# Kernel tuning notes

Hardware: AMD Instinct MI355X
Metric: run time of the kernel (lower is better)

## Reference

```python
import jax, jax.numpy as jnp
import numpy as np

N = 50000      # nodes
F_IN = 512     # input features
HID = 128      # hidden
CLS = 64       # classes
E = 800000     # edges (avg degree 16)
EPS = 1e-5


def setup_inputs() -> dict:
    key = jax.random.key(0)
    k = jax.random.split(key, 6)
    x = jax.random.normal(k[0], (N, F_IN), jnp.float32)
    edge_index = jax.random.randint(k[1], (2, E), 0, N, dtype=jnp.int32)
    W1 = jax.random.normal(k[2], (F_IN, HID), jnp.float32) / np.float32(np.sqrt(F_IN))
    b1 = jnp.zeros((HID,), jnp.float32)
    W2 = jax.random.normal(k[3], (HID, CLS), jnp.float32) / np.float32(np.sqrt(HID))
    b2 = jnp.zeros((CLS,), jnp.float32)
    return {"x": x, "edge_index": edge_index, "W1": W1, "b1": b1, "W2": W2, "b2": b2}


def bin_active(x):
    # BinActive(scalar=True): per-node sign binarization scaled by mean |x| over features
    return jnp.sign(x) * jnp.mean(jnp.abs(x), axis=1, keepdims=True)


def bin_weight(w):
    # binarized weight with per-output-channel scaling (XNOR-style)
    return jnp.sign(w) * jnp.mean(jnp.abs(w), axis=0, keepdims=True)


def gcn_norm(edge_index, n):
    # add self-loops, symmetric D^-1/2 (A+I) D^-1/2 normalization (cached in original)
    loops = jnp.arange(n, dtype=edge_index.dtype)
    row = jnp.concatenate([edge_index[0], loops])  # source
    col = jnp.concatenate([edge_index[1], loops])  # target
    deg = jax.ops.segment_sum(jnp.ones(row.shape[0], jnp.float32), col, num_segments=n)
    dinv = jnp.where(deg > 0, jax.lax.rsqrt(jnp.maximum(deg, 1.0)), 0.0)
    return row, col, dinv[row] * dinv[col]


def bigcn_conv(x, W, b, row, col, norm, n):
    h = x @ bin_weight(W)                                   # [n, out]
    msg = norm[:, None] * h[row]                            # gather + scale, [E+n, out]
    return jax.ops.segment_sum(msg, col, num_segments=n) + b


def reference(x, edge_index, W1, b1, W2, b2):
    n = x.shape[0]
    # BatchNorm1d(affine=False), batch statistics (biased var)
    mu = jnp.mean(x, axis=0)
    var = jnp.var(x, axis=0)
    x = (x - mu) * jax.lax.rsqrt(var + EPS)
    row, col, norm = gcn_norm(edge_index, n)
    # layer loop: BinActive -> (dropout is identity in eval) -> BiGCNConv
    x = bigcn_conv(bin_active(x), W1, b1, row, col, norm, n)
    x = bigcn_conv(bin_active(x), W2, b2, row, col, norm, n)
    return jax.nn.log_softmax(x, axis=1)
```

## Files before the change

### kernel.cpp

```cpp
#include <hip/hip_runtime.h>

typedef unsigned long long u64;

#define F_IN 512
#define HID 128
#define CLS 64
#define EPS 1e-5f
#define NSB 512

__global__ __launch_bounds__(256) void prep_k(const float4* __restrict__ x4,
                                              float* __restrict__ psum,
                                              float* __restrict__ psq,
                                              int n, int rpb,
                                              const int* __restrict__ col,
                                              int* __restrict__ deg, int e, int nbdeg,
                                              const float* __restrict__ W1,
                                              u64* __restrict__ sig1,
                                              float* __restrict__ beta1,
                                              const float* __restrict__ W2,
                                              ulonglong2* __restrict__ sigw2,
                                              float* __restrict__ beta2) {
    __shared__ float red[256][9];
    int b = blockIdx.x;
    int tid = threadIdx.x;
    if (b < NSB) {
        int c4 = tid & 127;
        int half = tid >> 7;
        int r0 = b * rpb;
        int r1 = min(n, r0 + rpb);
        float s0=0.f,s1=0.f,s2=0.f,s3=0.f,q0=0.f,q1=0.f,q2=0.f,q3=0.f;
#pragma unroll 4
        for (int r = r0 + half; r < r1; r += 2) {
            float4 v = x4[(size_t)r * 128 + c4];
            s0 += v.x; q0 += v.x * v.x;
            s1 += v.y; q1 += v.y * v.y;
            s2 += v.z; q2 += v.z * v.z;
            s3 += v.w; q3 += v.w * v.w;
        }
        red[tid][0]=s0; red[tid][1]=s1; red[tid][2]=s2; red[tid][3]=s3;
        red[tid][4]=q0; red[tid][5]=q1; red[tid][6]=q2; red[tid][7]=q3;
        __syncthreads();
        if (half == 0) {
            int c = c4 * 4;
            float* os = &psum[(size_t)b * 512 + c];
            float* oq = &psq [(size_t)b * 512 + c];
            os[0] = s0 + red[c4+128][0]; os[1] = s1 + red[c4+128][1];
            os[2] = s2 + red[c4+128][2]; os[3] = s3 + red[c4+128][3];
            oq[0] = q0 + red[c4+128][4]; oq[1] = q1 + red[c4+128][5];
            oq[2] = q2 + red[c4+128][6]; oq[3] = q3 + red[c4+128][7];
        }
    } else if (b < NSB + nbdeg) {
        int i = (b - NSB) * 256 + tid;
        if (i < e) atomicAdd(&deg[col[i]], 1);
    } else if (b < NSB + nbdeg + 32) {
        int wave = tid >> 6, l = tid & 63;
        int j = (b - NSB - nbdeg) * 4 + wave;
        float asum = 0.f;
#pragma unroll
        for (int jw = 0; jw < 8; ++jw) {
            int f = (jw < 4) ? (4*l + jw) : (256 + 4*l + (jw - 4));
            float v = W1[(size_t)f * HID + j];
            asum += fabsf(v);
            u64 bb = __ballot(v > 0.0f);
            if (l == 0) sig1[jw * HID + j] = bb;
        }
        for (int m = 32; m >= 1; m >>= 1) asum += __shfl_xor(asum, m);
        if (l == 0) beta1[j] = asum * (1.0f / 512.0f);
    } else {
        int wave = tid >> 6, l = tid & 63;
        int j = (b - NSB - nbdeg - 32) * 4 + wave;
        float v0 = W2[(size_t)(2 * l) * CLS + j];
        float v1 = W2[(size_t)(2 * l + 1) * CLS + j];
        float asum = fabsf(v0) + fabsf(v1);
        u64 s0 = __ballot(v0 > 0.0f);
        u64 s1 = __ballot(v1 > 0.0f);
        for (int m = 32; m >= 1; m >>= 1) asum += __shfl_xor(asum, m);
        if (l == 0) {
            ulonglong2 t; t.x = s0; t.y = s1;
            sigw2[j] = t;
            beta2[j] = asum * (1.0f / 128.0f);
        }
    }
}

__global__ __launch_bounds__(256) void mid_k(const float* __restrict__ psum,
                                             const float* __restrict__ psq,
                                             float* __restrict__ mu,
                                             float* __restrict__ rinv, int n,
                                             const int* __restrict__ deg,
                                             int* __restrict__ bsum) {
    __shared__ float reds[256], redq[256];
    __shared__ int lds[256];
    int b = blockIdx.x;
    int t = threadIdx.x;
    if (b < 16) {
        int cc = t & 31;
        int bs = t >> 5;
        int c = b * 32 + cc;
        float s = 0.f, q = 0.f;
#pragma unroll 4
        for (int p = bs; p < NSB; p += 8) {
            s += psum[(size_t)p * 512 + c];
            q += psq [(size_t)p * 512 + c];
        }
        reds[t] = s; redq[t] = q;
        __syncthreads();
        if (bs == 0) {
#pragma unroll
            for (int u = 1; u < 8; ++u) { s += reds[cc + 32*u]; q += redq[cc + 32*u]; }
            float m = s / (float)n;
            float v = q / (float)n - m * m;
            mu[c] = m;
            rinv[c] = rsqrtf(v + EPS);
        }
    } else {
        int blk = b - 16;
        int i = blk * 256 + t;
        lds[t] = (i < n) ? deg[i] : 0;
        __syncthreads();
        for (int s = 128; s > 0; s >>= 1) {
            if (t < s) lds[t] += lds[t + s];
            __syncthreads();
        }
        if (t == 0) bsum[blk] = lds[0];
    }
}

__global__ __launch_bounds__(256) void scan_bsum_k(const int* __restrict__ bsum,
                                                   int* __restrict__ boff, int nb) {
    __shared__ int lds[256];
    int t = threadIdx.x;
    int v = (t < nb) ? bsum[t] : 0;
    lds[t] = v;
    __syncthreads();
    for (int s = 1; s < 256; s <<= 1) {
        int add = (t >= s) ? lds[t - s] : 0;
        __syncthreads();
        lds[t] += add;
        __syncthreads();
    }
    if (t < nb) boff[t] = lds[t] - v;
}

__global__ __launch_bounds__(256) void scan_final_k(const int* __restrict__ deg,
                                                    const int* __restrict__ boff,
                                                    int* __restrict__ offs,
                                                    int* __restrict__ cursor,
                                                    float* __restrict__ dinv, int n) {
    __shared__ int lds[256];
    int t = threadIdx.x;
    int i = blockIdx.x * 256 + t;
    int v = (i < n) ? deg[i] : 0;
    lds[t] = v;
    __syncthreads();
    for (int s = 1; s < 256; s <<= 1) {
        int add = (t >= s) ? lds[t - s] : 0;
        __syncthreads();
        lds[t] += add;
        __syncthreads();
    }
    int excl = lds[t] - v + boff[blockIdx.x];
    if (i < n) {
        offs[i] = excl; cursor[i] = excl;
        dinv[i] = rsqrtf((float)v + 1.0f);
    }
}

__global__ __launch_bounds__(256) void main1_k(const float4* __restrict__ x4,
                                               const float4* __restrict__ mu4,
                                               const float4* __restrict__ rinv4,
                                               const u64* __restrict__ sigW,
                                               float* __restrict__ a1,
                                               short2* __restrict__ dots, int n, int nbin,
                                               const int* __restrict__ row,
                                               const int* __restrict__ col,
                                               const float* __restrict__ dinv,
                                               int* __restrict__ cursor,
                                               int2* __restrict__ csr, int e) {
    int b = blockIdx.x;
    int tid = threadIdx.x;
    if (b < nbin) {
        int wave = tid >> 6, l = tid & 63;
        int i = b * 4 + wave;
        if (i >= n) return;
        const float4* xr = x4 + (size_t)i * 128;
        float4 va = xr[l], vb = xr[64 + l];
        float4 ma = mu4[l], mb = mu4[64 + l];
        float4 ra = rinv4[l], rb = rinv4[64 + l];
        float t0 = va.x - ma.x, t1 = va.y - ma.y, t2 = va.z - ma.z, t3 = va.w - ma.w;
        float t4 = vb.x - mb.x, t5 = vb.y - mb.y, t6 = vb.z - mb.z, t7 = vb.w - mb.w;
        float asum = fabsf(t0)*ra.x + fabsf(t1)*ra.y + fabsf(t2)*ra.z + fabsf(t3)*ra.w
                   + fabsf(t4)*rb.x + fabsf(t5)*rb.y + fabsf(t6)*rb.z + fabsf(t7)*rb.w;
        u64 sx[8];
        sx[0] = __ballot(t0 > 0.f); sx[1] = __ballot(t1 > 0.f);
        sx[2] = __ballot(t2 > 0.f); sx[3] = __ballot(t3 > 0.f);
        sx[4] = __ballot(t4 > 0.f); sx[5] = __ballot(t5 > 0.f);
        sx[6] = __ballot(t6 > 0.f); sx[7] = __ballot(t7 > 0.f);
        for (int m = 32; m >= 1; m >>= 1) asum += __shfl_xor(asum, m);
        if (l == 0) a1[i] = asum * (1.0f / 512.0f);
        int c0 = 0, c1 = 0;
#pragma unroll
        for (int w = 0; w < 8; ++w) {
            c0 += __popcll(sx[w] ^ sigW[w * HID + 2*l]);
            c1 += __popcll(sx[w] ^ sigW[w * HID + 2*l + 1]);
        }
        dots[(size_t)i * 64 + l] = make_short2((short)(512 - 2*c0), (short)(512 - 2*c1));
    } else {
        int i = (b - nbin) * 256 + tid;
        if (i < e) {
            int r = row[i], c = col[i];
            int p = atomicAdd(&cursor[c], 1);
            float w = dinv[r] * dinv[c];
            csr[p] = make_int2(r, __float_as_int(w));
        }
    }
}

__global__ __launch_bounds__(256) void agg1_fused_k(const short2* __restrict__ dots,
                                                    const float* __restrict__ a1,
                                                    const int2* __restrict__ csr,
                                                    const int* __restrict__ offs,
                                                    const int* __restrict__ deg,
                                                    const float* __restrict__ dinv,
                                                    const float2* __restrict__ beta1_2,
                                                    const float2* __restrict__ b1_2,
                                                    u64* __restrict__ sig2x,
                                                    float* __restrict__ a2v, int n) {
    int tid = threadIdx.x;
    int wave = tid >> 6, l = tid & 63;
    int i = blockIdx.x * 4 + wave;
    if (i >= n) return;
    float di = dinv[i];
    float ts = di * di * a1[i];
    short2 ds = dots[(size_t)i * 64 + l];
    float acc0 = ts * (float)ds.x;
    float acc1 = ts * (float)ds.y;
    int off = offs[i], d = deg[i];
    int k = 0;
    for (; k + 8 <= d; k += 8) {
        int2 ee[8]; float tt[8]; short2 dd[8];
#pragma unroll
        for (int u = 0; u < 8; ++u) ee[u] = csr[off + k + u];
#pragma unroll
        for (int u = 0; u < 8; ++u) tt[u] = __int_as_float(ee[u].y) * a1[ee[u].x];
#pragma unroll
        for (int u = 0; u < 8; ++u) dd[u] = dots[(size_t)ee[u].x * 64 + l];
#pragma unroll
        for (int u = 0; u < 8; ++u) {
            acc0 += tt[u] * (float)dd[u].x;
            acc1 += tt[u] * (float)dd[u].y;
        }
    }
    for (; k < d; ++k) {
        int2 ew = csr[off + k];
        float t = __int_as_float(ew.y) * a1[ew.x];
        short2 dv = dots[(size_t)ew.x * 64 + l];
        acc0 += t * (float)dv.x;
        acc1 += t * (float)dv.y;
    }
    float2 be = beta1_2[l], bb = b1_2[l];
    acc0 = be.x * acc0 + bb.x;
    acc1 = be.y * acc1 + bb.y;
    float asum = fabsf(acc0) + fabsf(acc1);
    for (int m = 32; m >= 1; m >>= 1) asum += __shfl_xor(asum, m);
    u64 s0 = __ballot(acc0 > 0.f);
    u64 s1 = __ballot(acc1 > 0.f);
    if (l == 0) {
        ulonglong2 pk; pk.x = s0; pk.y = s1;
        *(ulonglong2*)&sig2x[2 * (size_t)i] = pk;
        a2v[i] = asum * (1.0f / 128.0f);
    }
}

__global__ __launch_bounds__(256) void agg2_pop_k(const u64* __restrict__ sig2x,
                                                  const float* __restrict__ a2v,
                                                  const int2* __restrict__ csr,
                                                  const int* __restrict__ offs,
                                                  const int* __restrict__ deg,
                                                  const float* __restrict__ dinv,
                                                  const ulonglong2* __restrict__ sigw2,
                                                  const float* __restrict__ beta2,
                                                  const float* __restrict__ b2,
                                                  float* __restrict__ out, int n) {
    int tid = threadIdx.x;
    int wave = tid >> 6, l = tid & 63;
    int i = blockIdx.x * 4 + wave;
    if (i >= n) return;
    ulonglong2 wsig = sigw2[l];
    float bet = beta2[l], bias = b2[l];
    float di = dinv[i];
    float ts = di * di * a2v[i];
    ulonglong2 ss = *(const ulonglong2*)&sig2x[2 * (size_t)i];
    int dp = __popcll(ss.x ^ wsig.x) + __popcll(ss.y ^ wsig.y);
    float acc = ts * (float)(128 - 2 * dp);
    int off = offs[i], d = deg[i];
    int k = 0;
    for (; k + 8 <= d; k += 8) {
        int2 ee[8]; float tt[8]; ulonglong2 gg[8];
#pragma unroll
        for (int u = 0; u < 8; ++u) ee[u] = csr[off + k + u];
#pragma unroll
        for (int u = 0; u < 8; ++u) tt[u] = __int_as_float(ee[u].y) * a2v[ee[u].x];
#pragma unroll
        for (int u = 0; u < 8; ++u) gg[u] = *(const ulonglong2*)&sig2x[2 * (size_t)ee[u].x];
#pragma unroll
        for (int u = 0; u < 8; ++u) {
            int p = __popcll(gg[u].x ^ wsig.x) + __popcll(gg[u].y ^ wsig.y);
            acc += tt[u] * (float)(128 - 2 * p);
        }
    }
    for (; k < d; ++k) {
        int2 ew = csr[off + k];
        ulonglong2 gs = *(const ulonglong2*)&sig2x[2 * (size_t)ew.x];
        float t = __int_as_float(ew.y) * a2v[ew.x];
        int p = __popcll(gs.x ^ wsig.x) + __popcll(gs.y ^ wsig.y);
        acc += t * (float)(128 - 2 * p);
    }
    float o = bet * acc + bias;
    float m = o;
    for (int k2 = 32; k2 >= 1; k2 >>= 1) m = fmaxf(m, __shfl_xor(m, k2));
    float ev = __expf(o - m);
    float s = ev;
    for (int k2 = 32; k2 >= 1; k2 >>= 1) s += __shfl_xor(s, k2);
    out[(size_t)i * CLS + l] = o - m - __logf(s);
}

extern "C" void kernel_launch(void* const* d_in, const int* in_sizes, int n_in,
                              void* d_out, int out_size, void* d_ws, size_t ws_size,
                              hipStream_t stream) {
    const float* x  = (const float*)d_in[0];
    const int*   ei = (const int*)d_in[1];
    const float* W1 = (const float*)d_in[2];
    const float* b1 = (const float*)d_in[3];
    const float* W2 = (const float*)d_in[4];
    const float* b2 = (const float*)d_in[5];
    float* out = (float*)d_out;

    const int n = in_sizes[0] / F_IN;
    const int e = in_sizes[1] / 2;
    const int* row = ei;
    const int* col = ei + e;

    char* w = (char*)d_ws;
    size_t off = 0;
    auto alloc = [&](size_t bytes) {
        void* p = w + off;
        off += (bytes + 255) & ~(size_t)255;
        return p;
    };
    int*   deg    = (int*)alloc((size_t)n * 4);
    size_t zero_bytes = off;
    float* psum   = (float*)alloc((size_t)NSB * 512 * 4);
    float* psq    = (float*)alloc((size_t)NSB * 512 * 4);
    float* mu     = (float*)alloc(F_IN * 4);
    float* rinv   = (float*)alloc(F_IN * 4);
    float* dinv   = (float*)alloc((size_t)n * 4);
    float* beta1  = (float*)alloc(HID * 4);
    u64*   sig1   = (u64*)alloc(HID * 8 * 8);
    ulonglong2* sigw2 = (ulonglong2*)alloc(CLS * 16);
    float* beta2  = (float*)alloc(CLS * 4);
    int*   offs   = (int*)alloc((size_t)n * 4);
    int*   cursor = (int*)alloc((size_t)n * 4);
    int*   bsum   = (int*)alloc(256 * 4);
    int*   boff   = (int*)alloc(256 * 4);
    int2*  csr    = (int2*)alloc((size_t)e * 8);
    short2* dots  = (short2*)alloc((size_t)n * 64 * 4);
    float* a1     = (float*)alloc((size_t)n * 4);
    u64*   sig2x  = (u64*)alloc((size_t)n * 2 * 8);
    float* a2v    = (float*)alloc((size_t)n * 4);
    (void)ws_size;

    hipMemsetAsync(deg, 0, zero_bytes, stream);

    int rpb = (n + NSB - 1) / NSB;
    int nbdeg = (e + 255) / 256;
    int nb = (n + 255) / 256;
    int nbin = (n + 3) / 4;

    prep_k<<<NSB + nbdeg + 32 + 16, 256, 0, stream>>>(
        (const float4*)x, psum, psq, n, rpb,
        col, deg, e, nbdeg,
        W1, sig1, beta1, W2, sigw2, beta2);

    mid_k<<<16 + nb, 256, 0, stream>>>(psum, psq, mu, rinv, n, deg, bsum);
    scan_bsum_k<<<1, 256, 0, stream>>>(bsum, boff, nb);
    scan_final_k<<<nb, 256, 0, stream>>>(deg, boff, offs, cursor, dinv, n);

    main1_k<<<nbin + nbdeg, 256, 0, stream>>>(
        (const float4*)x, (const float4*)mu, (const float4*)rinv, sig1, a1, dots, n, nbin,
        row, col, dinv, cursor, csr, e);

    agg1_fused_k<<<nbin, 256, 0, stream>>>(dots, a1, csr, offs, deg, dinv,
                                           (const float2*)beta1, (const float2*)b1,
                                           sig2x, a2v, n);
    agg2_pop_k<<<nbin, 256, 0, stream>>>(sig2x, a2v, csr, offs, deg, dinv,
                                         sigw2, beta2, b2, out, n);
}
```

Baseline: 360.8 us.

## Fold dinv into per-node scale, shrink CSR to int indices, vectorize edge loops

The symmetric normalization dinv[r]*dinv[c] is factored out. The source factor is folded into the per-node scale arrays (pa1/pa2), and the target factor is applied once after aggregation. Because of this the CSR stores only source indices as 4-byte ints instead of int2 pairs, which halves edge-list traffic in both aggregation passes. Degree counting and CSR fill now process four edges per thread with int4 loads, and degree is read from offs[i+1]-offs[i]. The risk is a small change in floating-point rounding order and an extra offs entry written by scan_final_k.

```diff
diff --git a/kernel.cpp b/kernel.cpp
--- a/kernel.cpp
+++ b/kernel.cpp
@@ -50,8 +50,17 @@
             oq[2] = q2 + red[c4+128][6]; oq[3] = q3 + red[c4+128][7];
         }
     } else if (b < NSB + nbdeg) {
-        int i = (b - NSB) * 256 + tid;
-        if (i < e) atomicAdd(&deg[col[i]], 1);
+        int i4 = (b - NSB) * 256 + tid;
+        int base = i4 * 4;
+        if (base + 3 < e) {
+            int4 cc = *(const int4*)&col[base];
+            atomicAdd(&deg[cc.x], 1);
+            atomicAdd(&deg[cc.y], 1);
+            atomicAdd(&deg[cc.z], 1);
+            atomicAdd(&deg[cc.w], 1);
+        } else {
+            for (int i = base; i < e; ++i) atomicAdd(&deg[col[i]], 1);
+        }
     } else if (b < NSB + nbdeg + 32) {
         int wave = tid >> 6, l = tid & 63;
         int j = (b - NSB - nbdeg) * 4 + wave;
@@ -163,6 +172,8 @@
     if (i < n) {
         offs[i] = excl; cursor[i] = excl;
         dinv[i] = rsqrtf((float)v + 1.0f);
+    } else if (i == n) {
+        offs[n] = excl;
     }
 }
 
@@ -170,13 +181,13 @@
                                                const float4* __restrict__ mu4,
                                                const float4* __restrict__ rinv4,
                                                const u64* __restrict__ sigW,
-                                               float* __restrict__ a1,
+                                               const float* __restrict__ dinv,
+                                               float* __restrict__ pa1,
                                                short2* __restrict__ dots, int n, int nbin,
                                                const int* __restrict__ row,
                                                const int* __restrict__ col,
-                                               const float* __restrict__ dinv,
                                                int* __restrict__ cursor,
-                                               int2* __restrict__ csr, int e) {
+                                               int* __restrict__ csr, int e) {
     int b = blockIdx.x;
     int tid = threadIdx.x;
     if (b < nbin) {
@@ -197,7 +208,7 @@
         sx[4] = __ballot(t4 > 0.f); sx[5] = __ballot(t5 > 0.f);
         sx[6] = __ballot(t6 > 0.f); sx[7] = __ballot(t7 > 0.f);
         for (int m = 32; m >= 1; m >>= 1) asum += __shfl_xor(asum, m);
-        if (l == 0) a1[i] = asum * (1.0f / 512.0f);
+        if (l == 0) pa1[i] = dinv[i] * asum * (1.0f / 512.0f);
         int c0 = 0, c1 = 0;
 #pragma unroll
         for (int w = 0; w < 8; ++w) {
@@ -206,45 +217,51 @@
         }
         dots[(size_t)i * 64 + l] = make_short2((short)(512 - 2*c0), (short)(512 - 2*c1));
     } else {
-        int i = (b - nbin) * 256 + tid;
-        if (i < e) {
-            int r = row[i], c = col[i];
-            int p = atomicAdd(&cursor[c], 1);
-            float w = dinv[r] * dinv[c];
-            csr[p] = make_int2(r, __float_as_int(w));
+        int i4 = (b - nbin) * 256 + tid;
+        int base = i4 * 4;
+        if (base + 3 < e) {
+            int4 rr = *(const int4*)&row[base];
+            int4 cc = *(const int4*)&col[base];
+            csr[atomicAdd(&cursor[cc.x], 1)] = rr.x;
+            csr[atomicAdd(&cursor[cc.y], 1)] = rr.y;
+            csr[atomicAdd(&cursor[cc.z], 1)] = rr.z;
+            csr[atomicAdd(&cursor[cc.w], 1)] = rr.w;
+        } else {
+            for (int i = base; i < e; ++i)
+                csr[atomicAdd(&cursor[col[i]], 1)] = row[i];
         }
     }
 }
 
 __global__ __launch_bounds__(256) void agg1_fused_k(const short2* __restrict__ dots,
-                                                    const float* __restrict__ a1,
-                                                    const int2* __restrict__ csr,
+                                                    const float* __restrict__ pa1,
+                                                    const int* __restrict__ csr,
                                                     const int* __restrict__ offs,
-                                                    const int* __restrict__ deg,
                                                     const float* __restrict__ dinv,
                                                     const float2* __restrict__ beta1_2,
                                                     const float2* __restrict__ b1_2,
                                                     u64* __restrict__ sig2x,
-                                                    float* __restrict__ a2v, int n) {
+                                                    float* __restrict__ pa2, int n) {
     int tid = threadIdx.x;
     int wave = tid >> 6, l = tid & 63;
     int i = blockIdx.x * 4 + wave;
     if (i >= n) return;
     float di = dinv[i];
-    float ts = di * di * a1[i];
     short2 ds = dots[(size_t)i * 64 + l];
-    float acc0 = ts * (float)ds.x;
-    float acc1 = ts * (float)ds.y;
-    int off = offs[i], d = deg[i];
+    float p_i = pa1[i];
+    float acc0 = p_i * (float)ds.x;
+    float acc1 = p_i * (float)ds.y;
+    int off = offs[i];
+    int d = offs[i + 1] - off;
     int k = 0;
     for (; k + 8 <= d; k += 8) {
-        int2 ee[8]; float tt[8]; short2 dd[8];
-#pragma unroll
-        for (int u = 0; u < 8; ++u) ee[u] = csr[off + k + u];
-#pragma unroll
-        for (int u = 0; u < 8; ++u) tt[u] = __int_as_float(ee[u].y) * a1[ee[u].x];
-#pragma unroll
-        for (int u = 0; u < 8; ++u) dd[u] = dots[(size_t)ee[u].x * 64 + l];
+        int rr[8]; float tt[8]; short2 dd[8];
+#pragma unroll
+        for (int u = 0; u < 8; ++u) rr[u] = csr[off + k + u];
+#pragma unroll
+        for (int u = 0; u < 8; ++u) tt[u] = pa1[rr[u]];
+#pragma unroll
+        for (int u = 0; u < 8; ++u) dd[u] = dots[(size_t)rr[u] * 64 + l];
 #pragma unroll
         for (int u = 0; u < 8; ++u) {
             acc0 += tt[u] * (float)dd[u].x;
@@ -252,15 +269,15 @@
         }
     }
     for (; k < d; ++k) {
-        int2 ew = csr[off + k];
-        float t = __int_as_float(ew.y) * a1[ew.x];
-        short2 dv = dots[(size_t)ew.x * 64 + l];
+        int r = csr[off + k];
+        float t = pa1[r];
+        short2 dv = dots[(size_t)r * 64 + l];
         acc0 += t * (float)dv.x;
         acc1 += t * (float)dv.y;
     }
     float2 be = beta1_2[l], bb = b1_2[l];
-    acc0 = be.x * acc0 + bb.x;
-    acc1 = be.y * acc1 + bb.y;
+    acc0 = be.x * (di * acc0) + bb.x;
+    acc1 = be.y * (di * acc1) + bb.y;
     float asum = fabsf(acc0) + fabsf(acc1);
     for (int m = 32; m >= 1; m >>= 1) asum += __shfl_xor(asum, m);
     u64 s0 = __ballot(acc0 > 0.f);
@@ -268,15 +285,14 @@
     if (l == 0) {
         ulonglong2 pk; pk.x = s0; pk.y = s1;
         *(ulonglong2*)&sig2x[2 * (size_t)i] = pk;
-        a2v[i] = asum * (1.0f / 128.0f);
+        pa2[i] = di * asum * (1.0f / 128.0f);
     }
 }
 
 __global__ __launch_bounds__(256) void agg2_pop_k(const u64* __restrict__ sig2x,
-                                                  const float* __restrict__ a2v,
-                                                  const int2* __restrict__ csr,
+                                                  const float* __restrict__ pa2,
+                                                  const int* __restrict__ csr,
                                                   const int* __restrict__ offs,
-                                                  const int* __restrict__ deg,
                                                   const float* __restrict__ dinv,
                                                   const ulonglong2* __restrict__ sigw2,
                                                   const float* __restrict__ beta2,
@@ -289,20 +305,21 @@
     ulonglong2 wsig = sigw2[l];
     float bet = beta2[l], bias = b2[l];
     float di = dinv[i];
-    float ts = di * di * a2v[i];
+    float p_i = pa2[i];
     ulonglong2 ss = *(const ulonglong2*)&sig2x[2 * (size_t)i];
     int dp = __popcll(ss.x ^ wsig.x) + __popcll(ss.y ^ wsig.y);
-    float acc = ts * (float)(128 - 2 * dp);
-    int off = offs[i], d = deg[i];
+    float acc = p_i * (float)(128 - 2 * dp);
+    int off = offs[i];
+    int d = offs[i + 1] - off;
     int k = 0;
     for (; k + 8 <= d; k += 8) {
-        int2 ee[8]; float tt[8]; ulonglong2 gg[8];
-#pragma unroll
-        for (int u = 0; u < 8; ++u) ee[u] = csr[off + k + u];
-#pragma unroll
-        for (int u = 0; u < 8; ++u) tt[u] = __int_as_float(ee[u].y) * a2v[ee[u].x];
-#pragma unroll
-        for (int u = 0; u < 8; ++u) gg[u] = *(const ulonglong2*)&sig2x[2 * (size_t)ee[u].x];
+        int rr[8]; float tt[8]; ulonglong2 gg[8];
+#pragma unroll
+        for (int u = 0; u < 8; ++u) rr[u] = csr[off + k + u];
+#pragma unroll
+        for (int u = 0; u < 8; ++u) tt[u] = pa2[rr[u]];
+#pragma unroll
+        for (int u = 0; u < 8; ++u) gg[u] = *(const ulonglong2*)&sig2x[2 * (size_t)rr[u]];
 #pragma unroll
         for (int u = 0; u < 8; ++u) {
             int p = __popcll(gg[u].x ^ wsig.x) + __popcll(gg[u].y ^ wsig.y);
@@ -310,13 +327,13 @@
         }
     }
     for (; k < d; ++k) {
-        int2 ew = csr[off + k];
-        ulonglong2 gs = *(const ulonglong2*)&sig2x[2 * (size_t)ew.x];
-        float t = __int_as_float(ew.y) * a2v[ew.x];
+        int r = csr[off + k];
+        ulonglong2 gs = *(const ulonglong2*)&sig2x[2 * (size_t)r];
+        float t = pa2[r];
         int p = __popcll(gs.x ^ wsig.x) + __popcll(gs.y ^ wsig.y);
         acc += t * (float)(128 - 2 * p);
     }
-    float o = bet * acc + bias;
+    float o = bet * (di * acc) + bias;
     float m = o;
     for (int k2 = 32; k2 >= 1; k2 >>= 1) m = fmaxf(m, __shfl_xor(m, k2));
     float ev = __expf(o - m);
@@ -359,21 +376,22 @@
     u64*   sig1   = (u64*)alloc(HID * 8 * 8);
     ulonglong2* sigw2 = (ulonglong2*)alloc(CLS * 16);
     float* beta2  = (float*)alloc(CLS * 4);
-    int*   offs   = (int*)alloc((size_t)n * 4);
+    int*   offs   = (int*)alloc(((size_t)n + 1) * 4);
     int*   cursor = (int*)alloc((size_t)n * 4);
     int*   bsum   = (int*)alloc(256 * 4);
     int*   boff   = (int*)alloc(256 * 4);
-    int2*  csr    = (int2*)alloc((size_t)e * 8);
+    int*   csr    = (int*)alloc((size_t)e * 4);
     short2* dots  = (short2*)alloc((size_t)n * 64 * 4);
-    float* a1     = (float*)alloc((size_t)n * 4);
+    float* pa1    = (float*)alloc((size_t)n * 4);
     u64*   sig2x  = (u64*)alloc((size_t)n * 2 * 8);
-    float* a2v    = (float*)alloc((size_t)n * 4);
+    float* pa2    = (float*)alloc((size_t)n * 4);
     (void)ws_size;
 
     hipMemsetAsync(deg, 0, zero_bytes, stream);
 
     int rpb = (n + NSB - 1) / NSB;
-    int nbdeg = (e + 255) / 256;
+    int e4 = (e + 3) / 4;
+    int nbdeg = (e4 + 255) / 256;
     int nb = (n + 255) / 256;
     int nbin = (n + 3) / 4;
 
@@ -387,12 +405,13 @@
     scan_final_k<<<nb, 256, 0, stream>>>(deg, boff, offs, cursor, dinv, n);
 
     main1_k<<<nbin + nbdeg, 256, 0, stream>>>(
-        (const float4*)x, (const float4*)mu, (const float4*)rinv, sig1, a1, dots, n, nbin,
-        row, col, dinv, cursor, csr, e);
-
-    agg1_fused_k<<<nbin, 256, 0, stream>>>(dots, a1, csr, offs, deg, dinv,
+        (const float4*)x, (const float4*)mu, (const float4*)rinv, sig1,
+        dinv, pa1, dots, n, nbin,
+        row, col, cursor, csr, e);
+
+    agg1_fused_k<<<nbin, 256, 0, stream>>>(dots, pa1, csr, offs, dinv,
                                            (const float2*)beta1, (const float2*)b1,
-                                           sig2x, a2v, n);
-    agg2_pop_k<<<nbin, 256, 0, stream>>>(sig2x, a2v, csr, offs, deg, dinv,
+                                           sig2x, pa2, n);
+    agg2_pop_k<<<nbin, 256, 0, stream>>>(sig2x, pa2, csr, offs, dinv,
                                          sigw2, beta2, b2, out, n);
 }
```

Measured after the change: 365.3 us. No clear change (+1.2%).
